# Performance work log

Measured on AMD Instinct MI355X. Metric: run time of the kernel, lower is better.

## Reference

```python
import jax, jax.numpy as jnp
import numpy as np

K = 1024
H = 16
HID = 4 * K
EPS = 1e-5


def _layernorm(x, g, b):
    mu = jnp.mean(x, axis=-1, keepdims=True)
    var = jnp.var(x, axis=-1, keepdims=True)
    return (x - mu) * jax.lax.rsqrt(var + EPS) * g + b


def _attention(xq, xkv, wq, wk, wv, wo, bo, causal):
    b, t, e = xq.shape
    tc = xkv.shape[1]
    h, s = H, e // H
    scale = e ** (-0.25)  # applied to both q and k, as in the original
    q = (xq @ wq).reshape(b, t, h, s) * scale
    k = (xkv @ wk).reshape(b, tc, h, s) * scale
    v = (xkv @ wv).reshape(b, tc, h, s)
    dot = jnp.einsum('bqhs,bkhs->bhqk', q, k)  # (b,h,t,tc)
    if causal:
        mask = jnp.tril(jnp.ones((t, tc), dtype=bool))
        dot = jnp.where(mask, dot, jnp.finfo(dot.dtype).min)
    att = jax.nn.softmax(dot, axis=-1)
    out = jnp.einsum('bhqk,bkhs->bqhs', att, v).reshape(b, t, e)
    return out @ wo + bo


def setup_inputs() -> dict:
    key = jax.random.key(0)
    ks = jax.random.split(key, 16)
    sd = K ** -0.5
    inp = {
        'x': jax.random.normal(ks[0], (4, 1024, K), jnp.float32),
        'context': jax.random.normal(ks[1], (4, 1024, K), jnp.float32),
        'sa_wq': jax.random.normal(ks[2], (K, K), jnp.float32) * sd,
        'sa_wk': jax.random.normal(ks[3], (K, K), jnp.float32) * sd,
        'sa_wv': jax.random.normal(ks[4], (K, K), jnp.float32) * sd,
        'sa_wo': jax.random.normal(ks[5], (K, K), jnp.float32) * sd,
        'sa_bo': jnp.zeros((K,), jnp.float32),
        'ca_wq': jax.random.normal(ks[6], (K, K), jnp.float32) * sd,
        'ca_wk': jax.random.normal(ks[7], (K, K), jnp.float32) * sd,
        'ca_wv': jax.random.normal(ks[8], (K, K), jnp.float32) * sd,
        'ca_wo': jax.random.normal(ks[9], (K, K), jnp.float32) * sd,
        'ca_bo': jnp.zeros((K,), jnp.float32),
        'n1_g': jnp.ones((K,), jnp.float32), 'n1_b': jnp.zeros((K,), jnp.float32),
        'n2_g': jnp.ones((K,), jnp.float32), 'n2_b': jnp.zeros((K,), jnp.float32),
        'n3_g': jnp.ones((K,), jnp.float32), 'n3_b': jnp.zeros((K,), jnp.float32),
        'ff_w1': jax.random.normal(ks[10], (K, HID), jnp.float32) * sd,
        'ff_b1': jnp.zeros((HID,), jnp.float32),
        'ff_w2': jax.random.normal(ks[11], (HID, K), jnp.float32) * (HID ** -0.5),
        'ff_b2': jnp.zeros((K,), jnp.float32),
    }
    return inp


def reference(x, context, sa_wq, sa_wk, sa_wv, sa_wo, sa_bo,
              ca_wq, ca_wk, ca_wv, ca_wo, ca_bo,
              n1_g, n1_b, n2_g, n2_b, n3_g, n3_b,
              ff_w1, ff_b1, ff_w2, ff_b2):
    # Masked self-attention + residual + LN (dropout is identity in eval mode)
    sa = _attention(x, x, sa_wq, sa_wk, sa_wv, sa_wo, sa_bo, causal=True)
    x = _layernorm(x + sa, n1_g, n1_b)
    # Cross-attention + residual + LN
    ca = _attention(x, context, ca_wq, ca_wk, ca_wv, ca_wo, ca_bo, causal=False)
    x = _layernorm(x + ca, n2_g, n2_b)
    # FFN + residual + LN
    ff = jax.nn.relu(x @ ff_w1 + ff_b1) @ ff_w2 + ff_b2
    x = _layernorm(x + ff, n3_g, n3_b)
    return x
```

## Files before the change

kernel.cpp:

```cpp
#include <hip/hip_runtime.h>

typedef __bf16 bf16x8 __attribute__((ext_vector_type(8)));
typedef __bf16 bf16x4 __attribute__((ext_vector_type(4)));
typedef float floatx4 __attribute__((ext_vector_type(4)));

#define EMB 1024
#define MROWS 4096
#define HIDN 4096
#define PSTRIDE ((size_t)MROWS * EMB)

struct TJobs { const float* s[16]; __bf16* d[16]; int sld[16]; int dld[16]; };
__global__ void transpose_cast16_kernel(TJobs a) {
    __shared__ float tile[32][33];
    int jz = blockIdx.z;
    const float* in = a.s[jz];
    __bf16* out = a.d[jz];
    int sld = a.sld[jz], dld = a.dld[jz];
    int tx = threadIdx.x, ty = threadIdx.y;
    int c0 = blockIdx.x * 32, r0 = blockIdx.y * 32;
#pragma unroll
    for (int i = 0; i < 32; i += 8)
        tile[ty + i][tx] = in[(size_t)(r0 + ty + i) * sld + c0 + tx];
    __syncthreads();
#pragma unroll
    for (int i = 0; i < 32; i += 8)
        out[(size_t)(c0 + ty + i) * dld + r0 + tx] = (__bf16)tile[tx][ty + i];
}

__global__ void transpose_v_kernel(const __bf16* __restrict__ in,
                                   __bf16* __restrict__ vt, int ld, int Tc) {
    __shared__ __bf16 tile[32][33];
    int tx = threadIdx.x, ty = threadIdx.y;
    int t0 = blockIdx.x * 32, s0 = blockIdx.y * 32;
    int bh = blockIdx.z, b = bh >> 4, h = bh & 15;
#pragma unroll
    for (int i = 0; i < 32; i += 8)
        tile[ty + i][tx] = in[(size_t)(b * Tc + t0 + ty + i) * ld + h * 64 + s0 + tx];
    __syncthreads();
#pragma unroll
    for (int i = 0; i < 32; i += 8)
        vt[((size_t)bh * 64 + s0 + ty + i) * Tc + t0 + tx] = tile[tx][ty + i];
}

__global__ void cast_bf16_kernel(const float* __restrict__ in,
                                 __bf16* __restrict__ out, int n) {
    int i = (blockIdx.x * 256 + threadIdx.x) * 4;
    if (i >= n) return;
    float4 v = *(const float4*)(in + i);
    bf16x4 o;
    o[0] = (__bf16)v.x; o[1] = (__bf16)v.y; o[2] = (__bf16)v.z; o[3] = (__bf16)v.w;
    *(bf16x4*)(out + i) = o;
}

template <int RELU>
__launch_bounds__(256, 4)
__global__ void gemm_bt(const __bf16* __restrict__ A, const __bf16* __restrict__ A2,
                        int asplit, const __bf16* __restrict__ Bt,
                        __bf16* __restrict__ cb, __bf16* __restrict__ cbalt,
                        const float* __restrict__ bias,
                        int M, int N, int Kd, float scale0, float scale1,
                        int split, int fx, int fy) {
    __shared__ alignas(16) __bf16 smem[2 * 128 * 32];
    __bf16* As = smem;
    __bf16* Bs = smem + 128 * 32;
    int tid  = threadIdx.x;
    int wv   = tid >> 6, lane = tid & 63;

    int L   = blockIdx.x + gridDim.x * (blockIdx.y + gridDim.y * blockIdx.z);
    int xcd = L & 7, j = L >> 3;
    int ff  = fx * fy;
    int zw  = xcd / ff;
    int rr  = xcd % ff;
    int nxf = gridDim.x / fx;
    int bnw = (j % nxf) * fx + (rr % fx);
    int bmw = (j / nxf) * fy + (rr / fx);
    int bn  = bnw * 128, bm = bmw * 128;

    int wm   = (wv & 1) * 64, wn = (wv >> 1) * 64;
    int l16  = lane & 15, g16 = lane >> 4;

    int kc   = Kd / gridDim.z;
    int zoff = zw * kc;

    const __bf16* Ause = (bn >= asplit) ? A2 : A;

    const __bf16* ag0 = Ause + (size_t)(bm + (tid >> 2)) * Kd + zoff + (tid & 3) * 8;
    const __bf16* ag1 = ag0 + (size_t)64 * Kd;
    const __bf16* bg0 = Bt + (size_t)(bn + (tid >> 2)) * Kd + zoff + (tid & 3) * 8;
    const __bf16* bg1 = bg0 + (size_t)64 * Kd;
    __bf16* al0 = &As[tid * 8];
    __bf16* al1 = &As[2048 + tid * 8];
    __bf16* bl0 = &Bs[tid * 8];
    __bf16* bl1 = &Bs[2048 + tid * 8];

    floatx4 acc[4][4] = {};

    bf16x8 pa0 = *(const bf16x8*)ag0;
    bf16x8 pa1 = *(const bf16x8*)ag1;
    bf16x8 pb0 = *(const bf16x8*)bg0;
    bf16x8 pb1 = *(const bf16x8*)bg1;

    for (int k0 = 0; k0 < kc; k0 += 32) {
        *(bf16x8*)al0 = pa0;
        *(bf16x8*)al1 = pa1;
        *(bf16x8*)bl0 = pb0;
        *(bf16x8*)bl1 = pb1;
        if (k0 + 32 < kc) {
            ag0 += 32; ag1 += 32; bg0 += 32; bg1 += 32;
            pa0 = *(const bf16x8*)ag0;
            pa1 = *(const bf16x8*)ag1;
            pb0 = *(const bf16x8*)bg0;
            pb1 = *(const bf16x8*)bg1;
        }
        __syncthreads();
        bf16x8 af[4], bfr[4];
#pragma unroll
        for (int i = 0; i < 4; ++i)
            af[i] = *(const bf16x8*)&As[(wm + i * 16 + l16) * 32 + g16 * 8];
#pragma unroll
        for (int jj = 0; jj < 4; ++jj)
            bfr[jj] = *(const bf16x8*)&Bs[(wn + jj * 16 + l16) * 32 + g16 * 8];
#pragma unroll
        for (int i = 0; i < 4; ++i)
#pragma unroll
            for (int jj = 0; jj < 4; ++jj)
                acc[i][jj] = __builtin_amdgcn_mfma_f32_16x16x32_bf16(af[i], bfr[jj], acc[i][jj], 0, 0, 0);
        __syncthreads();
    }

    __bf16* Cp = (zw == 0) ? cb : cbalt + (size_t)(zw - 1) * M * N;
    const float* bz = (zw == 0) ? bias : nullptr;

    __bf16* eb = smem + wv * 2048;
    int erow = lane >> 2;
    int ecol = (lane & 3) * 16;
#pragma unroll
    for (int i = 0; i < 4; ++i) {
#pragma unroll
        for (int jj = 0; jj < 4; ++jj) {
            int col  = bn + wn + jj * 16 + l16;
            float sc = (col < split) ? scale0 : scale1;
            float bv = bz ? bz[col] : 0.f;
#pragma unroll
            for (int r = 0; r < 4; ++r) {
                float v = acc[i][jj][r] * sc + bv;
                if (RELU) v = fmaxf(v, 0.f);
                eb[(g16 * 4 + r) * 76 + jj * 16 + l16] = (__bf16)v;
            }
        }
        bf16x8 t0 = *(const bf16x8*)&eb[erow * 76 + ecol];
        bf16x8 t1 = *(const bf16x8*)&eb[erow * 76 + ecol + 8];
        size_t gb = (size_t)(bm + wm + i * 16 + erow) * N + bn + wn + ecol;
        *(bf16x8*)&Cp[gb]     = t0;
        *(bf16x8*)&Cp[gb + 8] = t1;
    }
}

__launch_bounds__(256, 4)
__global__ void attn_kernel(const __bf16* __restrict__ qb, const __bf16* __restrict__ kb,
                            const __bf16* __restrict__ vt, int ldq, int ldk,
                            __bf16* __restrict__ out, int causal, int Tc) {
    constexpr int T = 1024;
    __shared__ alignas(16) __bf16 Qs[64 * 72];
    __shared__ alignas(16) __bf16 Ks[64 * 72];
    __shared__ alignas(16) __bf16 Vs[64 * 72];
    __shared__ alignas(16) __bf16 Ps[4][16 * 72];

    int tid = threadIdx.x;
    int wv = tid >> 6, lane = tid & 63;
    int l16 = lane & 15, g16 = lane >> 4;

    int L = blockIdx.x;
    int xcd = L & 7, idx = L >> 3;
    int i4 = idx & 15;
    int qt = ((i4 & 1) << 3) | ((i4 & 2) << 1) | ((i4 & 4) >> 1) | ((i4 & 8) >> 3);
    int pair = xcd + 8 * (idx >> 4);
    int h = pair & 15, b = pair >> 4;

    int r0 = tid >> 3, s8 = (tid & 7) * 8;
    int r1 = r0 + 32;

    {
        bf16x8 qv0 = *(const bf16x8*)(qb + (size_t)(b * T + qt * 64 + r0) * ldq + h * 64 + s8);
        bf16x8 qv1 = *(const bf16x8*)(qb + (size_t)(b * T + qt * 64 + r1) * ldq + h * 64 + s8);
        *(bf16x8*)&Qs[r0 * 72 + s8] = qv0;
        *(bf16x8*)&Qs[r1 * 72 + s8] = qv1;
    }

    floatx4 oacc[4] = {};
    float li = 0.f;

    int ktmax = causal ? (qt + 1) : (Tc / 64);

    const __bf16* kbase = kb + (size_t)b * Tc * ldk + h * 64 + s8;
    const __bf16* vbase = vt + (size_t)(b * 16 + h) * 64 * Tc + s8;

    bf16x8 kc0 = *(const bf16x8*)(kbase + (size_t)r0 * ldk);
    bf16x8 kc1 = *(const bf16x8*)(kbase + (size_t)r1 * ldk);
    bf16x8 vc0 = *(const bf16x8*)(vbase + (size_t)r0 * Tc);
    bf16x8 vc1 = *(const bf16x8*)(vbase + (size_t)r1 * Tc);
    bf16x8 kn0, kn1, vn0, vn1;

    for (int kt = 0; kt < ktmax; ++kt) {
        __syncthreads();
        *(bf16x8*)&Ks[r0 * 72 + s8] = kc0;
        *(bf16x8*)&Ks[r1 * 72 + s8] = kc1;
        *(bf16x8*)&Vs[r0 * 72 + s8] = vc0;
        *(bf16x8*)&Vs[r1 * 72 + s8] = vc1;
        if (kt + 1 < ktmax) {
            const __bf16* kp = kbase + (size_t)(kt + 1) * 64 * ldk;
            const __bf16* vp = vbase + (size_t)(kt + 1) * 64;
            kn0 = *(const bf16x8*)(kp + (size_t)r0 * ldk);
            kn1 = *(const bf16x8*)(kp + (size_t)r1 * ldk);
            vn0 = *(const bf16x8*)(vp + (size_t)r0 * Tc);
            vn1 = *(const bf16x8*)(vp + (size_t)r1 * Tc);
        }
        __syncthreads();

        floatx4 sacc[4] = {};
#pragma unroll
        for (int kk = 0; kk < 2; ++kk) {
            bf16x8 bq = *(const bf16x8*)&Qs[(wv * 16 + l16) * 72 + kk * 32 + g16 * 8];
#pragma unroll
            for (int j = 0; j < 4; ++j) {
                bf16x8 ak = *(const bf16x8*)&Ks[(j * 16 + l16) * 72 + kk * 32 + g16 * 8];
                sacc[j] = __builtin_amdgcn_mfma_f32_16x16x32_bf16(ak, bq, sacc[j], 0, 0, 0);
            }
        }
        if (causal && kt == qt) {
            int qloc = wv * 16 + l16;
#pragma unroll
            for (int j = 0; j < 4; ++j)
#pragma unroll
                for (int r = 0; r < 4; ++r)
                    if (j * 16 + g16 * 4 + r > qloc) sacc[j][r] = -1e30f;
        }

#pragma unroll
        for (int j = 0; j < 4; ++j) {
            bf16x4 pk;
#pragma unroll
            for (int r = 0; r < 4; ++r) {
                float p = __builtin_amdgcn_exp2f(sacc[j][r]);
                li += p;
                pk[r] = (__bf16)p;
            }
            *(bf16x4*)&Ps[wv][l16 * 72 + j * 16 + g16 * 4] = pk;
        }
#pragma unroll
        for (int kk = 0; kk < 2; ++kk) {
            bf16x8 bp = *(const bf16x8*)&Ps[wv][l16 * 72 + kk * 32 + g16 * 8];
#pragma unroll
            for (int j = 0; j < 4; ++j) {
                bf16x8 av = *(const bf16x8*)&Vs[(j * 16 + l16) * 72 + kk * 32 + g16 * 8];
                oacc[j] = __builtin_amdgcn_mfma_f32_16x16x32_bf16(av, bp, oacc[j], 0, 0, 0);
            }
        }
        kc0 = kn0; kc1 = kn1; vc0 = vn0; vc1 = vn1;
    }

    li += __shfl_xor(li, 16);
    li += __shfl_xor(li, 32);

    __syncthreads();
    float inv = 1.f / li;
#pragma unroll
    for (int j = 0; j < 4; ++j) {
        bf16x4 ok;
#pragma unroll
        for (int r = 0; r < 4; ++r) ok[r] = (__bf16)(oacc[j][r] * inv);
        *(bf16x4*)&Ks[(wv * 16 + l16) * 72 + j * 16 + g16 * 4] = ok;
    }
    int rw = lane >> 2, c4 = (lane & 3) * 16;
    bf16x8 o0 = *(const bf16x8*)&Ks[(wv * 16 + rw) * 72 + c4];
    bf16x8 o1 = *(const bf16x8*)&Ks[(wv * 16 + rw) * 72 + c4 + 8];
    size_t ob = (size_t)(b * T + qt * 64 + wv * 16 + rw) * EMB + h * 64 + c4;
    *(bf16x8*)&out[ob]     = o0;
    *(bf16x8*)&out[ob + 8] = o1;
}

__launch_bounds__(256)
__global__ void ln_kernel(const float* __restrict__ res,
                          const __bf16* __restrict__ pb, int np,
                          const float* __restrict__ g, const float* __restrict__ be,
                          float* __restrict__ outf, __bf16* __restrict__ outb) {
    __shared__ float red[8];
    int row = blockIdx.x, tid = threadIdx.x;
    size_t base = (size_t)row * EMB;
    float4 v = ((const float4*)(res + base))[tid];
    for (int i = 0; i < np; ++i) {
        bf16x4 u = *(const bf16x4*)(pb + i * PSTRIDE + base + tid * 4);
        v.x += (float)u[0]; v.y += (float)u[1];
        v.z += (float)u[2]; v.w += (float)u[3];
    }
    float s  = v.x + v.y + v.z + v.w;
    float ss = v.x * v.x + v.y * v.y + v.z * v.z + v.w * v.w;
#pragma unroll
    for (int o = 1; o < 64; o <<= 1) { s += __shfl_xor(s, o); ss += __shfl_xor(ss, o); }
    if ((tid & 63) == 0) { red[(tid >> 6) * 2] = s; red[(tid >> 6) * 2 + 1] = ss; }
    __syncthreads();
    s  = red[0] + red[2] + red[4] + red[6];
    ss = red[1] + red[3] + red[5] + red[7];
    float mu  = s * (1.0f / 1024.0f);
    float var = ss * (1.0f / 1024.0f) - mu * mu;
    float rs  = rsqrtf(var + 1e-5f);
    float4 gg = ((const float4*)g)[tid];
    float4 bb = ((const float4*)be)[tid];
    float4 y;
    y.x = (v.x - mu) * rs * gg.x + bb.x;
    y.y = (v.y - mu) * rs * gg.y + bb.y;
    y.z = (v.z - mu) * rs * gg.z + bb.z;
    y.w = (v.w - mu) * rs * gg.w + bb.w;
    ((float4*)(outf + base))[tid] = y;
    if (outb) {
        bf16x4 o;
        o[0] = (__bf16)y.x; o[1] = (__bf16)y.y; o[2] = (__bf16)y.z; o[3] = (__bf16)y.w;
        *(bf16x4*)(outb + base + tid * 4) = o;
    }
}

extern "C" void kernel_launch(void* const* d_in, const int* in_sizes, int n_in,
                              void* d_out, int out_size, void* d_ws, size_t ws_size,
                              hipStream_t stream) {
    const float* x     = (const float*)d_in[0];
    const float* ctx   = (const float*)d_in[1];
    const float* sa_wq = (const float*)d_in[2];
    const float* sa_wk = (const float*)d_in[3];
    const float* sa_wv = (const float*)d_in[4];
    const float* sa_wo = (const float*)d_in[5];
    const float* sa_bo = (const float*)d_in[6];
    const float* ca_wq = (const float*)d_in[7];
    const float* ca_wk = (const float*)d_in[8];
    const float* ca_wv = (const float*)d_in[9];
    const float* ca_wo = (const float*)d_in[10];
    const float* ca_bo = (const float*)d_in[11];
    const float* n1_g = (const float*)d_in[12];
    const float* n1_b = (const float*)d_in[13];
    const float* n2_g = (const float*)d_in[14];
    const float* n2_b = (const float*)d_in[15];
    const float* n3_g = (const float*)d_in[16];
    const float* n3_b = (const float*)d_in[17];
    const float* ff_w1 = (const float*)d_in[18];
    const float* ff_b1 = (const float*)d_in[19];
    const float* ff_w2 = (const float*)d_in[20];
    const float* ff_b2 = (const float*)d_in[21];

    size_t off = 0;
    auto alloc = [&](size_t bytes) {
        void* p = (char*)d_ws + off;
        off += (bytes + 255) & ~(size_t)255;
        return p;
    };
    __bf16* w_sa_qkvT = (__bf16*)alloc((size_t)3 * EMB * EMB * 2);
    __bf16* w_sa_oT   = (__bf16*)alloc((size_t)EMB * EMB * 2);
    __bf16* w_ca_kvqT = (__bf16*)alloc((size_t)3 * EMB * EMB * 2);
    __bf16* w_ca_oT   = (__bf16*)alloc((size_t)EMB * EMB * 2);
    __bf16* w1T       = (__bf16*)alloc((size_t)HIDN * EMB * 2);
    __bf16* w2T       = (__bf16*)alloc((size_t)EMB * HIDN * 2);
    __bf16* xb        = (__bf16*)alloc((size_t)MROWS * EMB * 2);
    __bf16* qkv       = (__bf16*)alloc((size_t)MROWS * 3 * EMB * 2);
    __bf16* ao        = (__bf16*)alloc((size_t)MROWS * EMB * 2);
    __bf16* hid       = (__bf16*)alloc((size_t)MROWS * HIDN * 2);
    __bf16* x1b       = (__bf16*)alloc((size_t)MROWS * EMB * 2);
    __bf16* vt        = (__bf16*)alloc((size_t)MROWS * EMB * 2);
    float* res1       = (float*)alloc((size_t)MROWS * EMB * 4);
    float* res2       = (float*)alloc((size_t)MROWS * EMB * 4);

    __bf16* qkvc = qkv;
    __bf16* pbo  = qkv;
    __bf16* pbf  = xb;

    const float QSC = 0.04508422002778011f;
    const int   BIG = 1 << 30;
    dim3 tb(32, 8);

    TJobs tj;
    tj.s[0] = sa_wq; tj.d[0] = w_sa_qkvT;                          tj.sld[0] = EMB;  tj.dld[0] = EMB;
    tj.s[1] = sa_wk; tj.d[1] = w_sa_qkvT + (size_t)EMB * EMB;      tj.sld[1] = EMB;  tj.dld[1] = EMB;
    tj.s[2] = sa_wv; tj.d[2] = w_sa_qkvT + (size_t)2 * EMB * EMB;  tj.sld[2] = EMB;  tj.dld[2] = EMB;
    tj.s[3] = sa_wo; tj.d[3] = w_sa_oT;                            tj.sld[3] = EMB;  tj.dld[3] = EMB;
    tj.s[4] = ca_wk; tj.d[4] = w_ca_kvqT;                          tj.sld[4] = EMB;  tj.dld[4] = EMB;
    tj.s[5] = ca_wv; tj.d[5] = w_ca_kvqT + (size_t)EMB * EMB;      tj.sld[5] = EMB;  tj.dld[5] = EMB;
    tj.s[6] = ca_wq; tj.d[6] = w_ca_kvqT + (size_t)2 * EMB * EMB;  tj.sld[6] = EMB;  tj.dld[6] = EMB;
    tj.s[7] = ca_wo; tj.d[7] = w_ca_oT;                            tj.sld[7] = EMB;  tj.dld[7] = EMB;
    for (int c = 0; c < 4; ++c) {
        tj.s[8 + c] = ff_w1 + (size_t)c * 1024;
        tj.d[8 + c] = w1T + (size_t)c * 1024 * 1024;
        tj.sld[8 + c] = HIDN; tj.dld[8 + c] = EMB;
    }
    for (int c = 0; c < 4; ++c) {
        tj.s[12 + c] = ff_w2 + (size_t)c * 1024 * 1024;
        tj.d[12 + c] = w2T + (size_t)c * 1024;
        tj.sld[12 + c] = EMB; tj.dld[12 + c] = HIDN;
    }
    transpose_cast16_kernel<<<dim3(32, 32, 16), tb, 0, stream>>>(tj);

    cast_bf16_kernel<<<4096, 256, 0, stream>>>(x, xb, MROWS * EMB);
    gemm_bt<0><<<dim3(24, 32), 256, 0, stream>>>(xb, xb, BIG, w_sa_qkvT,
        qkv, nullptr, nullptr, MROWS, 3 * EMB, EMB, QSC, 1.f, 1024, 2, 4);
    transpose_v_kernel<<<dim3(32, 2, 64), tb, 0, stream>>>(qkv + 2 * EMB, vt, 3 * EMB, 1024);
    attn_kernel<<<1024, 256, 0, stream>>>(qkv, qkv + EMB, vt, 3 * EMB, 3 * EMB, ao, 1, 1024);
    gemm_bt<0><<<dim3(8, 32, 2), 256, 0, stream>>>(ao, ao, BIG, w_sa_oT,
        pbo, pbo + PSTRIDE, sa_bo, MROWS, EMB, EMB, 1.f, 1.f, 0, 2, 2);
    ln_kernel<<<4096, 256, 0, stream>>>(x, pbo, 2, n1_g, n1_b, res1, x1b);

    cast_bf16_kernel<<<4096, 256, 0, stream>>>(ctx, xb, MROWS * EMB);
    gemm_bt<0><<<dim3(24, 32), 256, 0, stream>>>(xb, x1b, 2048, w_ca_kvqT,
        qkvc, nullptr, nullptr, MROWS, 3 * EMB, EMB, 1.f, QSC, 2048, 2, 4);
    transpose_v_kernel<<<dim3(32, 2, 64), tb, 0, stream>>>(qkvc + EMB, vt, 3 * EMB, 1024);
    attn_kernel<<<1024, 256, 0, stream>>>(qkvc + 2 * EMB, qkvc, vt, 3 * EMB, 3 * EMB, ao, 0, 1024);
    gemm_bt<0><<<dim3(8, 32, 2), 256, 0, stream>>>(ao, ao, BIG, w_ca_oT,
        pbo, pbo + PSTRIDE, ca_bo, MROWS, EMB, EMB, 1.f, 1.f, 0, 2, 2);
    ln_kernel<<<4096, 256, 0, stream>>>(res1, pbo, 2, n2_g, n2_b, res2, x1b);

    gemm_bt<1><<<dim3(32, 32), 256, 0, stream>>>(x1b, x1b, BIG, w1T,
        hid, nullptr, ff_b1, MROWS, HIDN, EMB, 1.f, 1.f, 0, 2, 4);
    gemm_bt<0><<<dim3(8, 32, 4), 256, 0, stream>>>(hid, hid, BIG, w2T,
        pbf, pbf + PSTRIDE, ff_b2, MROWS, EMB, HIDN, 1.f, 1.f, 0, 1, 2);
    ln_kernel<<<4096, 256, 0, stream>>>(res2, pbf, 4, n3_g, n3_b, (float*)d_out, nullptr);
}
```

Measured before the change: 473.5 us.

## Use direct global-to-LDS loads in large GEMMs and 128-row query tiles in attention

Adds a non-register staging path to the GEMM that uses global_load_lds so tiles go straight into shared memory. The QKV and FFN1 GEMMs use it, while the split-K output GEMMs keep the register-prefetch path. The attention kernel now processes 128 query rows per block as two 64-row sub-tiles that share each K/V tile load, which halves the grid and the K/V traffic. The cost is a loss of register prefetch overlap in the LDS-load path, lower attention occupancy (launch bound 3), and fewer blocks to balance the causal work.

```diff
diff --git a/kernel.cpp b/kernel.cpp
--- a/kernel.cpp
+++ b/kernel.cpp
@@ -8,6 +8,12 @@
 #define MROWS 4096
 #define HIDN 4096
 #define PSTRIDE ((size_t)MROWS * EMB)
+
+__device__ __forceinline__ void load_lds16(const __bf16* g, __bf16* l) {
+    __builtin_amdgcn_global_load_lds(
+        (const __attribute__((address_space(1))) void*)g,
+        (__attribute__((address_space(3))) void*)l, 16, 0, 0);
+}
 
 struct TJobs { const float* s[16]; __bf16* d[16]; int sld[16]; int dld[16]; };
 __global__ void transpose_cast16_kernel(TJobs a) {
@@ -52,7 +58,7 @@
     *(bf16x4*)(out + i) = o;
 }
 
-template <int RELU>
+template <int RELU, int REG>
 __launch_bounds__(256, 4)
 __global__ void gemm_bt(const __bf16* __restrict__ A, const __bf16* __restrict__ A2,
                         int asplit, const __bf16* __restrict__ Bt,
@@ -95,36 +101,58 @@
 
     floatx4 acc[4][4] = {};
 
-    bf16x8 pa0 = *(const bf16x8*)ag0;
-    bf16x8 pa1 = *(const bf16x8*)ag1;
-    bf16x8 pb0 = *(const bf16x8*)bg0;
-    bf16x8 pb1 = *(const bf16x8*)bg1;
-
-    for (int k0 = 0; k0 < kc; k0 += 32) {
-        *(bf16x8*)al0 = pa0;
-        *(bf16x8*)al1 = pa1;
-        *(bf16x8*)bl0 = pb0;
-        *(bf16x8*)bl1 = pb1;
-        if (k0 + 32 < kc) {
+    if (REG) {
+        bf16x8 pa0 = *(const bf16x8*)ag0;
+        bf16x8 pa1 = *(const bf16x8*)ag1;
+        bf16x8 pb0 = *(const bf16x8*)bg0;
+        bf16x8 pb1 = *(const bf16x8*)bg1;
+        for (int k0 = 0; k0 < kc; k0 += 32) {
+            *(bf16x8*)al0 = pa0;
+            *(bf16x8*)al1 = pa1;
+            *(bf16x8*)bl0 = pb0;
+            *(bf16x8*)bl1 = pb1;
+            if (k0 + 32 < kc) {
+                ag0 += 32; ag1 += 32; bg0 += 32; bg1 += 32;
+                pa0 = *(const bf16x8*)ag0;
+                pa1 = *(const bf16x8*)ag1;
+                pb0 = *(const bf16x8*)bg0;
+                pb1 = *(const bf16x8*)bg1;
+            }
+            __syncthreads();
+            bf16x8 af[4], bfr[4];
+#pragma unroll
+            for (int i = 0; i < 4; ++i)
+                af[i] = *(const bf16x8*)&As[(wm + i * 16 + l16) * 32 + g16 * 8];
+#pragma unroll
+            for (int jj = 0; jj < 4; ++jj)
+                bfr[jj] = *(const bf16x8*)&Bs[(wn + jj * 16 + l16) * 32 + g16 * 8];
+#pragma unroll
+            for (int i = 0; i < 4; ++i)
+#pragma unroll
+                for (int jj = 0; jj < 4; ++jj)
+                    acc[i][jj] = __builtin_amdgcn_mfma_f32_16x16x32_bf16(af[i], bfr[jj], acc[i][jj], 0, 0, 0);
+            __syncthreads();
+        }
+    } else {
+        for (int k0 = 0; k0 < kc; k0 += 32) {
+            __syncthreads();
+            load_lds16(ag0, al0); load_lds16(ag1, al1);
+            load_lds16(bg0, bl0); load_lds16(bg1, bl1);
             ag0 += 32; ag1 += 32; bg0 += 32; bg1 += 32;
-            pa0 = *(const bf16x8*)ag0;
-            pa1 = *(const bf16x8*)ag1;
-            pb0 = *(const bf16x8*)bg0;
-            pb1 = *(const bf16x8*)bg1;
-        }
-        __syncthreads();
-        bf16x8 af[4], bfr[4];
-#pragma unroll
-        for (int i = 0; i < 4; ++i)
-            af[i] = *(const bf16x8*)&As[(wm + i * 16 + l16) * 32 + g16 * 8];
-#pragma unroll
-        for (int jj = 0; jj < 4; ++jj)
-            bfr[jj] = *(const bf16x8*)&Bs[(wn + jj * 16 + l16) * 32 + g16 * 8];
-#pragma unroll
-        for (int i = 0; i < 4; ++i)
+            __syncthreads();
+            bf16x8 af[4], bfr[4];
+#pragma unroll
+            for (int i = 0; i < 4; ++i)
+                af[i] = *(const bf16x8*)&As[(wm + i * 16 + l16) * 32 + g16 * 8];
 #pragma unroll
             for (int jj = 0; jj < 4; ++jj)
-                acc[i][jj] = __builtin_amdgcn_mfma_f32_16x16x32_bf16(af[i], bfr[jj], acc[i][jj], 0, 0, 0);
+                bfr[jj] = *(const bf16x8*)&Bs[(wn + jj * 16 + l16) * 32 + g16 * 8];
+#pragma unroll
+            for (int i = 0; i < 4; ++i)
+#pragma unroll
+                for (int jj = 0; jj < 4; ++jj)
+                    acc[i][jj] = __builtin_amdgcn_mfma_f32_16x16x32_bf16(af[i], bfr[jj], acc[i][jj], 0, 0, 0);
+        }
         __syncthreads();
     }
 
@@ -156,12 +184,12 @@
     }
 }
 
-__launch_bounds__(256, 4)
+__launch_bounds__(256, 3)
 __global__ void attn_kernel(const __bf16* __restrict__ qb, const __bf16* __restrict__ kb,
                             const __bf16* __restrict__ vt, int ldq, int ldk,
                             __bf16* __restrict__ out, int causal, int Tc) {
     constexpr int T = 1024;
-    __shared__ alignas(16) __bf16 Qs[64 * 72];
+    __shared__ alignas(16) __bf16 Qs[128 * 72];
     __shared__ alignas(16) __bf16 Ks[64 * 72];
     __shared__ alignas(16) __bf16 Vs[64 * 72];
     __shared__ alignas(16) __bf16 Ps[4][16 * 72];
@@ -172,25 +200,25 @@
 
     int L = blockIdx.x;
     int xcd = L & 7, idx = L >> 3;
-    int i4 = idx & 15;
-    int qt = ((i4 & 1) << 3) | ((i4 & 2) << 1) | ((i4 & 4) >> 1) | ((i4 & 8) >> 3);
-    int pair = xcd + 8 * (idx >> 4);
+    int i3 = idx & 7;
+    int qt2 = (idx & 32) ? (7 - i3) : i3;
+    int pair = xcd + 8 * (idx >> 3);
     int h = pair & 15, b = pair >> 4;
 
     int r0 = tid >> 3, s8 = (tid & 7) * 8;
     int r1 = r0 + 32;
 
-    {
-        bf16x8 qv0 = *(const bf16x8*)(qb + (size_t)(b * T + qt * 64 + r0) * ldq + h * 64 + s8);
-        bf16x8 qv1 = *(const bf16x8*)(qb + (size_t)(b * T + qt * 64 + r1) * ldq + h * 64 + s8);
-        *(bf16x8*)&Qs[r0 * 72 + s8] = qv0;
-        *(bf16x8*)&Qs[r1 * 72 + s8] = qv1;
-    }
-
-    floatx4 oacc[4] = {};
-    float li = 0.f;
-
-    int ktmax = causal ? (qt + 1) : (Tc / 64);
+#pragma unroll
+    for (int p = 0; p < 4; ++p) {
+        int row = r0 + p * 32;
+        bf16x8 qv = *(const bf16x8*)(qb + (size_t)(b * T + qt2 * 128 + row) * ldq + h * 64 + s8);
+        *(bf16x8*)&Qs[row * 72 + s8] = qv;
+    }
+
+    floatx4 oacc[2][4] = {};
+    float li[2] = {0.f, 0.f};
+
+    int ktend = causal ? (2 * qt2 + 2) : (Tc / 64);
 
     const __bf16* kbase = kb + (size_t)b * Tc * ldk + h * 64 + s8;
     const __bf16* vbase = vt + (size_t)(b * 16 + h) * 64 * Tc + s8;
@@ -201,13 +229,13 @@
     bf16x8 vc1 = *(const bf16x8*)(vbase + (size_t)r1 * Tc);
     bf16x8 kn0, kn1, vn0, vn1;
 
-    for (int kt = 0; kt < ktmax; ++kt) {
+    for (int kt = 0; kt < ktend; ++kt) {
         __syncthreads();
         *(bf16x8*)&Ks[r0 * 72 + s8] = kc0;
         *(bf16x8*)&Ks[r1 * 72 + s8] = kc1;
         *(bf16x8*)&Vs[r0 * 72 + s8] = vc0;
         *(bf16x8*)&Vs[r1 * 72 + s8] = vc1;
-        if (kt + 1 < ktmax) {
+        if (kt + 1 < ktend) {
             const __bf16* kp = kbase + (size_t)(kt + 1) * 64 * ldk;
             const __bf16* vp = vbase + (size_t)(kt + 1) * 64;
             kn0 = *(const bf16x8*)(kp + (size_t)r0 * ldk);
@@ -217,66 +245,74 @@
         }
         __syncthreads();
 
-        floatx4 sacc[4] = {};
-#pragma unroll
-        for (int kk = 0; kk < 2; ++kk) {
-            bf16x8 bq = *(const bf16x8*)&Qs[(wv * 16 + l16) * 72 + kk * 32 + g16 * 8];
+#pragma unroll
+        for (int sub = 0; sub < 2; ++sub) {
+            if (causal && kt > 2 * qt2 + sub) continue;
+
+            floatx4 sacc[4] = {};
+#pragma unroll
+            for (int kk = 0; kk < 2; ++kk) {
+                bf16x8 bq = *(const bf16x8*)&Qs[(sub * 64 + wv * 16 + l16) * 72 + kk * 32 + g16 * 8];
+#pragma unroll
+                for (int j = 0; j < 4; ++j) {
+                    bf16x8 ak = *(const bf16x8*)&Ks[(j * 16 + l16) * 72 + kk * 32 + g16 * 8];
+                    sacc[j] = __builtin_amdgcn_mfma_f32_16x16x32_bf16(ak, bq, sacc[j], 0, 0, 0);
+                }
+            }
+            if (causal && kt == 2 * qt2 + sub) {
+                int qloc = wv * 16 + l16;
+#pragma unroll
+                for (int j = 0; j < 4; ++j)
+#pragma unroll
+                    for (int r = 0; r < 4; ++r)
+                        if (j * 16 + g16 * 4 + r > qloc) sacc[j][r] = -1e30f;
+            }
+
 #pragma unroll
             for (int j = 0; j < 4; ++j) {
-                bf16x8 ak = *(const bf16x8*)&Ks[(j * 16 + l16) * 72 + kk * 32 + g16 * 8];
-                sacc[j] = __builtin_amdgcn_mfma_f32_16x16x32_bf16(ak, bq, sacc[j], 0, 0, 0);
-            }
-        }
-        if (causal && kt == qt) {
-            int qloc = wv * 16 + l16;
-#pragma unroll
-            for (int j = 0; j < 4; ++j)
-#pragma unroll
-                for (int r = 0; r < 4; ++r)
-                    if (j * 16 + g16 * 4 + r > qloc) sacc[j][r] = -1e30f;
-        }
-
+                bf16x4 pk;
+#pragma unroll
+                for (int r = 0; r < 4; ++r) {
+                    float p = __builtin_amdgcn_exp2f(sacc[j][r]);
+                    li[sub] += p;
+                    pk[r] = (__bf16)p;
+                }
+                *(bf16x4*)&Ps[wv][l16 * 72 + j * 16 + g16 * 4] = pk;
+            }
+#pragma unroll
+            for (int kk = 0; kk < 2; ++kk) {
+                bf16x8 bp = *(const bf16x8*)&Ps[wv][l16 * 72 + kk * 32 + g16 * 8];
+#pragma unroll
+                for (int j = 0; j < 4; ++j) {
+                    bf16x8 av = *(const bf16x8*)&Vs[(j * 16 + l16) * 72 + kk * 32 + g16 * 8];
+                    oacc[sub][j] = __builtin_amdgcn_mfma_f32_16x16x32_bf16(av, bp, oacc[sub][j], 0, 0, 0);
+                }
+            }
+        }
+        kc0 = kn0; kc1 = kn1; vc0 = vn0; vc1 = vn1;
+    }
+
+    li[0] += __shfl_xor(li[0], 16); li[0] += __shfl_xor(li[0], 32);
+    li[1] += __shfl_xor(li[1], 16); li[1] += __shfl_xor(li[1], 32);
+
+    __syncthreads();
+    int rw = lane >> 2, c4 = (lane & 3) * 16;
+#pragma unroll
+    for (int sub = 0; sub < 2; ++sub) {
+        float inv = 1.f / li[sub];
 #pragma unroll
         for (int j = 0; j < 4; ++j) {
-            bf16x4 pk;
-#pragma unroll
-            for (int r = 0; r < 4; ++r) {
-                float p = __builtin_amdgcn_exp2f(sacc[j][r]);
-                li += p;
-                pk[r] = (__bf16)p;
-            }
-            *(bf16x4*)&Ps[wv][l16 * 72 + j * 16 + g16 * 4] = pk;
-        }
-#pragma unroll
-        for (int kk = 0; kk < 2; ++kk) {
-            bf16x8 bp = *(const bf16x8*)&Ps[wv][l16 * 72 + kk * 32 + g16 * 8];
-#pragma unroll
-            for (int j = 0; j < 4; ++j) {
-                bf16x8 av = *(const bf16x8*)&Vs[(j * 16 + l16) * 72 + kk * 32 + g16 * 8];
-                oacc[j] = __builtin_amdgcn_mfma_f32_16x16x32_bf16(av, bp, oacc[j], 0, 0, 0);
-            }
-        }
-        kc0 = kn0; kc1 = kn1; vc0 = vn0; vc1 = vn1;
-    }
-
-    li += __shfl_xor(li, 16);
-    li += __shfl_xor(li, 32);
-
-    __syncthreads();
-    float inv = 1.f / li;
-#pragma unroll
-    for (int j = 0; j < 4; ++j) {
-        bf16x4 ok;
-#pragma unroll
-        for (int r = 0; r < 4; ++r) ok[r] = (__bf16)(oacc[j][r] * inv);
-        *(bf16x4*)&Ks[(wv * 16 + l16) * 72 + j * 16 + g16 * 4] = ok;
-    }
-    int rw = lane >> 2, c4 = (lane & 3) * 16;
-    bf16x8 o0 = *(const bf16x8*)&Ks[(wv * 16 + rw) * 72 + c4];
-    bf16x8 o1 = *(const bf16x8*)&Ks[(wv * 16 + rw) * 72 + c4 + 8];
-    size_t ob = (size_t)(b * T + qt * 64 + wv * 16 + rw) * EMB + h * 64 + c4;
-    *(bf16x8*)&out[ob]     = o0;
-    *(bf16x8*)&out[ob + 8] = o1;
+            bf16x4 ok;
+#pragma unroll
+            for (int r = 0; r < 4; ++r) ok[r] = (__bf16)(oacc[sub][j][r] * inv);
+            *(bf16x4*)&Ks[(wv * 16 + l16) * 72 + j * 16 + g16 * 4] = ok;
+        }
+        bf16x8 o0 = *(const bf16x8*)&Ks[(wv * 16 + rw) * 72 + c4];
+        bf16x8 o1 = *(const bf16x8*)&Ks[(wv * 16 + rw) * 72 + c4 + 8];
+        size_t ob = (size_t)(b * T + qt2 * 128 + sub * 64 + wv * 16 + rw) * EMB + h * 64 + c4;
+        *(bf16x8*)&out[ob]     = o0;
+        *(bf16x8*)&out[ob + 8] = o1;
+    }
 }
 
 __launch_bounds__(256)
@@ -396,26 +432,26 @@
     transpose_cast16_kernel<<<dim3(32, 32, 16), tb, 0, stream>>>(tj);
 
     cast_bf16_kernel<<<4096, 256, 0, stream>>>(x, xb, MROWS * EMB);
-    gemm_bt<0><<<dim3(24, 32), 256, 0, stream>>>(xb, xb, BIG, w_sa_qkvT,
+    gemm_bt<0, 0><<<dim3(24, 32), 256, 0, stream>>>(xb, xb, BIG, w_sa_qkvT,
         qkv, nullptr, nullptr, MROWS, 3 * EMB, EMB, QSC, 1.f, 1024, 2, 4);
     transpose_v_kernel<<<dim3(32, 2, 64), tb, 0, stream>>>(qkv + 2 * EMB, vt, 3 * EMB, 1024);
-    attn_kernel<<<1024, 256, 0, stream>>>(qkv, qkv + EMB, vt, 3 * EMB, 3 * EMB, ao, 1, 1024);
-    gemm_bt<0><<<dim3(8, 32, 2), 256, 0, stream>>>(ao, ao, BIG, w_sa_oT,
+    attn_kernel<<<512, 256, 0, stream>>>(qkv, qkv + EMB, vt, 3 * EMB, 3 * EMB, ao, 1, 1024);
+    gemm_bt<0, 1><<<dim3(8, 32, 2), 256, 0, stream>>>(ao, ao, BIG, w_sa_oT,
         pbo, pbo + PSTRIDE, sa_bo, MROWS, EMB, EMB, 1.f, 1.f, 0, 2, 2);
     ln_kernel<<<4096, 256, 0, stream>>>(x, pbo, 2, n1_g, n1_b, res1, x1b);
 
     cast_bf16_kernel<<<4096, 256, 0, stream>>>(ctx, xb, MROWS * EMB);
-    gemm_bt<0><<<dim3(24, 32), 256, 0, stream>>>(xb, x1b, 2048, w_ca_kvqT,
+    gemm_bt<0, 0><<<dim3(24, 32), 256, 0, stream>>>(xb, x1b, 2048, w_ca_kvqT,
         qkvc, nullptr, nullptr, MROWS, 3 * EMB, EMB, 1.f, QSC, 2048, 2, 4);
     transpose_v_kernel<<<dim3(32, 2, 64), tb, 0, stream>>>(qkvc + EMB, vt, 3 * EMB, 1024);
-    attn_kernel<<<1024, 256, 0, stream>>>(qkvc + 2 * EMB, qkvc, vt, 3 * EMB, 3 * EMB, ao, 0, 1024);
-    gemm_bt<0><<<dim3(8, 32, 2), 256, 0, stream>>>(ao, ao, BIG, w_ca_oT,
+    attn_kernel<<<512, 256, 0, stream>>>(qkvc + 2 * EMB, qkvc, vt, 3 * EMB, 3 * EMB, ao, 0, 1024);
+    gemm_bt<0, 1><<<dim3(8, 32, 2), 256, 0, stream>>>(ao, ao, BIG, w_ca_oT,
         pbo, pbo + PSTRIDE, ca_bo, MROWS, EMB, EMB, 1.f, 1.f, 0, 2, 2);
     ln_kernel<<<4096, 256, 0, stream>>>(res1, pbo, 2, n2_g, n2_b, res2, x1b);
 
-    gemm_bt<1><<<dim3(32, 32), 256, 0, stream>>>(x1b, x1b, BIG, w1T,
+    gemm_bt<1, 0><<<dim3(32, 32), 256, 0, stream>>>(x1b, x1b, BIG, w1T,
         hid, nullptr, ff_b1, MROWS, HIDN, EMB, 1.f, 1.f, 0, 2, 4);
-    gemm_bt<0><<<dim3(8, 32, 4), 256, 0, stream>>>(hid, hid, BIG, w2T,
+    gemm_bt<0, 1><<<dim3(8, 32, 4), 256, 0, stream>>>(hid, hid, BIG, w2T,
         pbf, pbf + PSTRIDE, ff_b2, MROWS, EMB, HIDN, 1.f, 1.f, 0, 1, 2);
     ln_kernel<<<4096, 256, 0, stream>>>(res2, pbf, 4, n3_g, n3_b, (float*)d_out, nullptr);
 }
```

Result: faster. 461.0 us (-2.6%).
